# Kernel optimization log

Measured on AMD Instinct MI355X. Metric: run time of the kernel, lower is better.

Reference implementation:

```python
import jax, jax.numpy as jnp
import numpy as np

BN_EPS = 1e-5

def _bn_train(x, g, b):
    # BatchNorm1d in training mode: biased batch stats over the row dim
    m = x.mean(0)
    v = x.var(0)
    return g * (x - m) * jax.lax.rsqrt(v + BN_EPS) + b


def setup_inputs() -> dict:
    key = jax.random.key(0)
    ks = jax.random.split(key, 16)
    N, V, C, H, T, NC, OD, EH, EC = 128, 128, 256, 512, 12, 5, 5, 256, 256
    s = 0.05
    idx = jax.random.randint(ks[1], (T, N), 0, NC)
    return {
        "x": jax.random.normal(ks[0], (N, V, C), jnp.float32),
        "hidden_states": jnp.zeros((N, V, H), jnp.float32),
        "cell_states": jnp.zeros((N, V, H), jnp.float32),
        "one_hots_c_pred_seq": jax.nn.one_hot(idx, NC, dtype=jnp.float32),
        "W_ih": jax.random.normal(ks[2], (4 * H, C), jnp.float32) * s,
        "W_hh": jax.random.normal(ks[3], (4 * H, H), jnp.float32) * s,
        "b_ih": jax.random.normal(ks[4], (4 * H,), jnp.float32) * s,
        "b_hh": jax.random.normal(ks[5], (4 * H,), jnp.float32) * s,
        "W_cls": jax.random.normal(ks[6], (NC, H), jnp.float32) * s,
        "b_cls": jax.random.normal(ks[7], (NC,), jnp.float32) * s,
        "W_eh": jax.random.normal(ks[8], (EH, H), jnp.float32) * s,
        "b_eh": jax.random.normal(ks[9], (EH,), jnp.float32) * s,
        "g_eh": jnp.ones((EH,), jnp.float32),
        "beta_eh": jnp.zeros((EH,), jnp.float32),
        "W_ec": jax.random.normal(ks[10], (EC, NC), jnp.float32) * s,
        "b_ec": jax.random.normal(ks[11], (EC,), jnp.float32) * s,
        "g_ec": jnp.ones((EC,), jnp.float32),
        "beta_ec": jnp.zeros((EC,), jnp.float32),
        "W_out": jax.random.normal(ks[12], (OD, EH + EC), jnp.float32) * s,
        "b_out": jax.random.normal(ks[13], (OD,), jnp.float32) * s,
    }


def reference(x, hidden_states, cell_states, one_hots_c_pred_seq,
              W_ih, W_hh, b_ih, b_hh, W_cls, b_cls,
              W_eh, b_eh, g_eh, beta_eh, W_ec, b_ec, g_ec, beta_ec,
              W_out, b_out):
    N, V, C = x.shape
    H = hidden_states.shape[-1]
    xf = x.reshape(N * V, C)
    gx = xf @ W_ih.T + b_ih  # input gates are identical every step (x is repeated)

    def step(carry, onehot):
        h, c = carry  # [N*V, H]
        gates = gx + h @ W_hh.T + b_hh
        i, f, g, o = jnp.split(gates, 4, axis=1)  # pytorch LSTMCell gate order
        c = jax.nn.sigmoid(f) * c + jax.nn.sigmoid(i) * jnp.tanh(g)
        h = jax.nn.sigmoid(o) * jnp.tanh(c)
        # ClassifierLayer: avg-pool over V then 1x1 conv == mean + linear
        oc = h.reshape(N, V, H).mean(1) @ W_cls.T + b_cls  # [N, nc]
        # PredictionLayer
        eh = jax.nn.relu(_bn_train(h @ W_eh.T + b_eh, g_eh, beta_eh))
        ohr = jnp.broadcast_to(onehot[:, None, :], (N, V, onehot.shape[-1])).reshape(N * V, -1)
        ec = jax.nn.relu(_bn_train(ohr @ W_ec.T + b_ec, g_ec, beta_ec))
        op = jnp.concatenate([eh, ec], axis=1) @ W_out.T + b_out  # [N*V, out_dim]
        return (h, c), (op.reshape(N, V, -1), oc)

    carry0 = (hidden_states.reshape(N * V, H), cell_states.reshape(N * V, H))
    _, (preds, c_outs) = jax.lax.scan(step, carry0, one_hots_c_pred_seq)
    preds = preds.transpose(1, 0, 2, 3)  # [N, T, V, out_dim]
    # output_activation: bivariate-Gaussian params
    pred_outs = jnp.stack([preds[..., 0], preds[..., 1],
                           jnp.exp(preds[..., 2]), jnp.exp(preds[..., 3]),
                           jnp.tanh(preds[..., 4])], axis=-1)
    return pred_outs, c_outs
```

## Files before the change

kernel.cpp:

```cpp
#include <hip/hip_runtime.h>
#include <hip/hip_bf16.h>
#include <stdint.h>

typedef __hip_bfloat16 bf16;
typedef __attribute__((ext_vector_type(8))) short bf16x8;
typedef __attribute__((ext_vector_type(4))) short bf16x4;
typedef __attribute__((ext_vector_type(4))) float f32x4;

#define NN 128
#define VV 128
#define CC 256
#define HH 512
#define TT 12
#define NCLS 5
#define OD 5
#define EHD 256
#define KCAT (HH + CC)
#define ROWS (NN * VV)
#define PRED_SZ (NN * TT * VV * OD)
#define LDP 72
#define MiB (1ull << 20)


__device__ __forceinline__ float sigm(float x) { return 1.f / (1.f + __expf(-x)); }
__device__ __forceinline__ float tanh_(float x) {
    x = fminf(fmaxf(x, -15.f), 15.f);
    float e = __expf(2.f * x);
    return (e - 1.f) / (e + 1.f);
}
__device__ __forceinline__ float bf2f(unsigned short v) {
    unsigned u = ((unsigned)v) << 16; float f; __builtin_memcpy(&f, &u, 4); return f;
}
__device__ __forceinline__ float ldin(const void* p, int i, int is32) {
    return is32 ? ((const float*)p)[i] : __bfloat162float(((const bf16*)p)[i]);
}

__global__ void detect_dtype(const void* g_eh, int* flag, int* hnz) {
    unsigned w = *(const unsigned*)g_eh;
    *flag = (w == 0x3F800000u) ? 1 : 0;
    *hnz = 0;
}

__global__ __launch_bounds__(256) void convert_in(const void* src, bf16* dst, int n, const int* flag) {
    int is32 = *flag;
    int i = blockIdx.x * 256 + threadIdx.x;
    int stride = gridDim.x * 256;
    if (is32) { const float* s = (const float*)src; for (; i < n; i += stride) dst[i] = __float2bfloat16(s[i]); }
    else      { const bf16*  s = (const bf16*)src;  for (; i < n; i += stride) dst[i] = s[i]; }
}

__global__ __launch_bounds__(256) void convert_in_hflag(const void* src, bf16* dst, int n, const int* flag,
                                                        int* nz) {
    int is32 = *flag;
    int i = blockIdx.x * 256 + threadIdx.x;
    int stride = gridDim.x * 256;
    int loc = 0;
    if (is32) {
        const float* s = (const float*)src;
        for (; i < n; i += stride) { float v = s[i]; if (__float_as_uint(v) != 0u) loc = 1; dst[i] = __float2bfloat16(v); }
    } else {
        const bf16* s = (const bf16*)src;
        for (; i < n; i += stride) { bf16 v = s[i]; if (*(const unsigned short*)&v) loc = 1; dst[i] = v; }
    }
    if (loc) atomicOr(nz, 1);
}

__global__ __launch_bounds__(256) void init_c(const void* cell, bf16* c, const int* flag) {
    int is32 = *flag;
    size_t i = (size_t)blockIdx.x * 256 + threadIdx.x;
    const size_t total = (size_t)ROWS * HH;
    for (; i < total; i += (size_t)8192 * 256) c[i] = __float2bfloat16(ldin(cell, (int)i, is32));
}

__device__ __forceinline__ void issue_loads(const bf16* __restrict__ A, int lda, int row0, int ka,
                                            const bf16* __restrict__ B, int ldb, int col0, int kb,
                                            bf16x8 ar[4], bf16x8 br[4]) {
    int tid = threadIdx.x;
#pragma unroll
    for (int it = 0; it < 4; ++it) {
        int cidx = tid + 256 * it;
        int row = cidx >> 3;
        int cc8 = (cidx & 7) * 8;
        ar[it] = *(const bf16x8*)(A + (size_t)(row0 + row) * lda + ka + cc8);
        br[it] = *(const bf16x8*)(B + (size_t)(col0 + row) * ldb + kb + cc8);
    }
}
__device__ __forceinline__ void write_lds(bf16* As, bf16* Bs, const bf16x8 ar[4], const bf16x8 br[4]) {
    int tid = threadIdx.x;
#pragma unroll
    for (int it = 0; it < 4; ++it) {
        int cidx = tid + 256 * it;
        int row = cidx >> 3;
        int cc8 = (cidx & 7) * 8;
        *(bf16x8*)(As + row * LDP + cc8) = ar[it];
        *(bf16x8*)(Bs + row * LDP + cc8) = br[it];
    }
}
__device__ __forceinline__ void tile_mfma(const bf16* As, const bf16* Bs, f32x4 acc[4][4]) {
    const int lane = threadIdx.x & 63, wave = threadIdx.x >> 6;
    const int wro = (wave >> 1) * 64, wco = (wave & 1) * 64;
    const int l15 = lane & 15, l8 = (lane >> 4) * 8;
#pragma unroll
    for (int kk = 0; kk < 64; kk += 32) {
        bf16x8 af[4], bg[4];
#pragma unroll
        for (int x = 0; x < 4; ++x) {
            af[x] = *(const bf16x8*)(As + (wro + x * 16 + l15) * LDP + kk + l8);
            bg[x] = *(const bf16x8*)(Bs + (wco + x * 16 + l15) * LDP + kk + l8);
        }
#pragma unroll
        for (int bi = 0; bi < 4; ++bi)
#pragma unroll
            for (int bj = 0; bj < 4; ++bj)
                acc[bi][bj] = __builtin_amdgcn_mfma_f32_16x16x32_bf16(af[bi], bg[bj], acc[bi][bj], 0, 0, 0);
    }
}

__global__ __launch_bounds__(256) void prep_weights(const void* __restrict__ Wih, const void* __restrict__ Whh,
                                                    const void* __restrict__ bih, const void* __restrict__ bhh,
                                                    bf16* __restrict__ Wihp, bf16* __restrict__ Whhp,
                                                    float* __restrict__ biasp, const int* flag) {
    int is32 = *flag;
    int jg = blockIdx.x;
    int b = jg >> 7, j = jg & 127;
    int gate = (j >> 4) & 3;
    int unit = b * 32 + (j & 15) + 16 * (j >> 6);
    int p = gate * HH + unit;
    for (int k = threadIdx.x; k < HH; k += 256)
        Whhp[(size_t)jg * HH + k] = __float2bfloat16(ldin(Whh, p * HH + k, is32));
    for (int k = threadIdx.x; k < CC; k += 256)
        Wihp[(size_t)jg * CC + k] = __float2bfloat16(ldin(Wih, p * CC + k, is32));
    if (threadIdx.x == 0)
        biasp[jg] = ldin(bih, p, is32) + ldin(bhh, p, is32);
}

__global__ __launch_bounds__(256) void gemm_k0(const bf16* __restrict__ A, const bf16* __restrict__ B,
                                               const float* __restrict__ biasp, bf16* __restrict__ gx) {
    __shared__ bf16 As[128 * LDP], Bs[128 * LDP];
    f32x4 acc[4][4] = {};
    bf16x8 ar[4], br[4];
    int row0 = blockIdx.x * 128, col0 = blockIdx.y * 128;
    issue_loads(A, CC, row0, 0, B, CC, col0, 0, ar, br);
    for (int k0 = 0; k0 < CC; k0 += 64) {
        __syncthreads();
        write_lds(As, Bs, ar, br);
        __syncthreads();
        int kn = k0 + 64;
        if (kn < CC) issue_loads(A, CC, row0, kn, B, CC, col0, kn, ar, br);
        tile_mfma(As, Bs, acc);
    }
    int lane = threadIdx.x & 63, wave = threadIdx.x >> 6;
    int wro = (wave >> 1) * 64, wco = (wave & 1) * 64;
    int l15 = lane & 15, lr4 = (lane >> 4) * 4;
#pragma unroll
    for (int bj = 0; bj < 4; ++bj) {
        int j = wco + bj * 16 + l15;
        float bia = biasp[col0 + j];
        int sidx = wco + l15 * 4 + bj;
#pragma unroll
        for (int bi = 0; bi < 4; ++bi)
#pragma unroll
            for (int reg = 0; reg < 4; ++reg) {
                int r = row0 + wro + bi * 16 + lr4 + reg;
                gx[(size_t)r * 2048 + col0 + sidx] = __float2bfloat16(acc[bi][bj][reg] + bia);
            }
    }
}

__global__ __launch_bounds__(256) void ec_precompute(const void* __restrict__ W_ec, const void* __restrict__ b_ec,
                                                     const void* __restrict__ g_ec, const void* __restrict__ beta_ec,
                                                     const void* __restrict__ W_out, const void* __restrict__ b_out,
                                                     const void* __restrict__ onehot, float* __restrict__ ecd_all,
                                                     const int* flag) {
    __shared__ float ecv[NCLS][EHD];
    __shared__ float cntf[NCLS];
    __shared__ float ecdc[NCLS][OD];
    int is32 = *flag;
    int t = blockIdx.x, tid = threadIdx.x;
    int ohoff = t * NN * NCLS;
    if (tid < NCLS) {
        float cnum = 0.f;
        for (int n = 0; n < NN; ++n) cnum += ldin(onehot, ohoff + n * NCLS + tid, is32);
        cntf[tid] = cnum * (1.f / NN);
    }
    __syncthreads();
    {
        int j = tid;
        float vals[NCLS];
        float m = 0.f, e2 = 0.f;
        float be = ldin(b_ec, j, is32);
        for (int cc = 0; cc < NCLS; ++cc) {
            vals[cc] = ldin(W_ec, j * NCLS + cc, is32) + be;
            m += cntf[cc] * vals[cc];
            e2 += cntf[cc] * vals[cc] * vals[cc];
        }
        float rs = rsqrtf(e2 - m * m + 1e-5f);
        float g = ldin(g_ec, j, is32), bt = ldin(beta_ec, j, is32);
        for (int cc = 0; cc < NCLS; ++cc)
            ecv[cc][j] = fmaxf(g * (vals[cc] - m) * rs + bt, 0.f);
    }
    __syncthreads();
    if (tid < NCLS * OD) {
        int cc = tid / OD, k = tid % OD;
        float s = 0.f;
        for (int j = 0; j < EHD; ++j) s += ecv[cc][j] * ldin(W_out, k * (EHD * 2) + EHD + j, is32);
        ecdc[cc][k] = s;
    }
    __syncthreads();
    if (tid < NN) {
        for (int k = 0; k < OD; ++k) {
            float s = ldin(b_out, k, is32);
            for (int cc = 0; cc < NCLS; ++cc) s += ldin(onehot, ohoff + tid * NCLS + cc, is32) * ecdc[cc][k];
            ecd_all[((size_t)t * NN + tid) * OD + k] = s;
        }
    }
}

__device__ __forceinline__ void final_rows(int grp, const bf16* __restrict__ ehp, const float* __restrict__ colsum,
                                           const float* __restrict__ colss, const void* __restrict__ g_eh,
                                           const void* __restrict__ beta_eh, const float* __restrict__ ecd_all,
                                           const float* Wl, void* __restrict__ out, int t, int is32) {
    int wave = threadIdx.x >> 6, lane = threadIdx.x & 63;
    int r = grp * 4 + wave;
    int j0 = lane * 4;
    float av[4], bv[4];
#pragma unroll
    for (int e = 0; e < 4; ++e) {
        float mean = colsum[j0 + e] * (1.f / ROWS);
        float var = colss[j0 + e] * (1.f / ROWS) - mean * mean;
        float a = ldin(g_eh, j0 + e, is32) * rsqrtf(var + 1e-5f);
        av[e] = a;
        bv[e] = ldin(beta_eh, j0 + e, is32) - mean * a;
    }
    bf16x4 xs = *(const bf16x4*)(ehp + (size_t)r * EHD + j0);
    float v0 = fmaxf(av[0] * bf2f((unsigned short)xs[0]) + bv[0], 0.f);
    float v1 = fmaxf(av[1] * bf2f((unsigned short)xs[1]) + bv[1], 0.f);
    float v2 = fmaxf(av[2] * bf2f((unsigned short)xs[2]) + bv[2], 0.f);
    float v3 = fmaxf(av[3] * bf2f((unsigned short)xs[3]) + bv[3], 0.f);
    float p[OD];
#pragma unroll
    for (int k = 0; k < OD; ++k)
        p[k] = v0 * Wl[k * EHD + j0] + v1 * Wl[k * EHD + j0 + 1] + v2 * Wl[k * EHD + j0 + 2] + v3 * Wl[k * EHD + j0 + 3];
#pragma unroll
    for (int off = 32; off; off >>= 1)
#pragma unroll
        for (int k = 0; k < OD; ++k) p[k] += __shfl_down(p[k], off, 64);
    if (lane == 0) {
        int n = r >> 7, v = r & 127;
        const float* en = ecd_all + ((size_t)t * NN + n) * OD;
        float o0 = p[0] + en[0];
        float o1 = p[1] + en[1];
        float o2 = expf(p[2] + en[2]);
        float o3 = expf(p[3] + en[3]);
        float o4 = tanh_(p[4] + en[4]);
        size_t base = (size_t)n * (TT * VV * OD) + (size_t)t * (VV * OD) + (size_t)v * OD;
        if (is32) {
            float* dst = (float*)out + base;
            dst[0] = o0; dst[1] = o1; dst[2] = o2; dst[3] = o3; dst[4] = o4;
        } else {
            bf16* dst = (bf16*)out + base;
            dst[0] = __float2bfloat16(o0);
            dst[1] = __float2bfloat16(o1);
            dst[2] = __float2bfloat16(o2);
            dst[3] = __float2bfloat16(o3);
            dst[4] = __float2bfloat16(o4);
        }
    }
}

__global__ __launch_bounds__(256) void lstm_fused(const bf16* __restrict__ h_in, const bf16* __restrict__ Whhp,
                                                  const bf16* __restrict__ gx, bf16* __restrict__ c,
                                                  bf16* __restrict__ h_out, float* __restrict__ csum_cur,
                                                  float* __restrict__ colsum_z, float* __restrict__ colss_z,
                                                  const bf16* __restrict__ Weh, const void* __restrict__ b_eh,
                                                  bf16* __restrict__ ehp_w, float* __restrict__ colsum_w,
                                                  float* __restrict__ colss_w, const float* __restrict__ csum_prev,
                                                  const void* __restrict__ W_cls, const void* __restrict__ b_cls,
                                                  void* __restrict__ outp, int t_aux,
                                                  const bf16* __restrict__ ehp_r, const float* __restrict__ colsum_r,
                                                  const float* __restrict__ colss_r, const void* __restrict__ g_eh,
                                                  const void* __restrict__ beta_eh, const void* __restrict__ W_out,
                                                  const float* __restrict__ ecd_all, int t_final,
                                                  const int* __restrict__ flag) {
    __shared__ __align__(16) unsigned char smem[37376];
    int tid = threadIdx.x;
    if (blockIdx.x < 2048) {
        bf16* As = (bf16*)smem;
        bf16* Bs = (bf16*)(smem + 128 * LDP * 2);
        float* hsum = (float*)(smem + 36864);
        f32x4 acc[4][4] = {};
        bf16x8 ar[4], br[4];
        bf16x4 gpre[16];
        unsigned short cpre[16];
        int row0 = (blockIdx.x & 127) * 128, col0 = (blockIdx.x >> 7) * 128;
        int lane = tid & 63, wave = tid >> 6;
        int wro = (wave >> 1) * 64;
        int l15 = lane & 15, lr4 = (lane >> 4) * 4;
        int ul = (wave & 1) * 16 + l15;
        int u = (blockIdx.x >> 7) * 32 + ul;
        const bf16* gxp = gx + col0 + (wave & 1) * 64 + l15 * 4;
        issue_loads(h_in, HH, row0, 0, Whhp, HH, col0, 0, ar, br);
#pragma unroll
        for (int k0 = 0; k0 < HH; k0 += 64) {
            __syncthreads();
            write_lds(As, Bs, ar, br);
            __syncthreads();
            int kn = k0 + 64;
            if (kn < HH) issue_loads(h_in, HH, row0, kn, Whhp, HH, col0, kn, ar, br);
#pragma unroll
            for (int e = 0; e < 2; ++e) {
                int idx = (k0 >> 6) * 2 + e;
                int bi = idx >> 2, reg = idx & 3;
                int r = row0 + wro + bi * 16 + lr4 + reg;
                gpre[idx] = *(const bf16x4*)(gxp + (size_t)r * 2048);
                cpre[idx] = *(const unsigned short*)(c + (size_t)r * HH + u);
            }
            tile_mfma(As, Bs, acc);
        }
        if (tid < 32) hsum[tid] = 0.f;
        if (blockIdx.x == 0) { colsum_z[tid] = 0.f; colss_z[tid] = 0.f; }
        __syncthreads();
        float hpart = 0.f;
#pragma unroll
        for (int bi = 0; bi < 4; ++bi) {
#pragma unroll
            for (int reg = 0; reg < 4; ++reg) {
                int idx = bi * 4 + reg;
                int r = row0 + wro + bi * 16 + lr4 + reg;
                float gi = acc[bi][0][reg] + bf2f((unsigned short)gpre[idx][0]);
                float gf = acc[bi][1][reg] + bf2f((unsigned short)gpre[idx][1]);
                float gg = acc[bi][2][reg] + bf2f((unsigned short)gpre[idx][2]);
                float go = acc[bi][3][reg] + bf2f((unsigned short)gpre[idx][3]);
                float iv = sigm(gi), fv = sigm(gf), gv = tanh_(gg), ov = sigm(go);
                size_t ci = (size_t)r * HH + u;
                float cn = fv * bf2f(cpre[idx]) + iv * gv;
                c[ci] = __float2bfloat16(cn);
                float hv = ov * tanh_(cn);
                h_out[ci] = __float2bfloat16(hv);
                hpart += hv;
            }
        }
        atomicAdd(&hsum[ul], hpart);
        __syncthreads();
        if (tid < 32) csum_cur[(size_t)(blockIdx.x & 127) * HH + (blockIdx.x >> 7) * 32 + tid] = hsum[tid];
        return;
    }
    int is32 = *flag;
    int b = blockIdx.x - 2048;
    if (b >= 640) {
        if (t_final < 0) return;
        float* Wl = (float*)smem;
        for (int i = tid; i < OD * EHD; i += 256)
            Wl[i] = ldin(W_out, (i >> 8) * (EHD * 2) + (i & 255), is32);
        __syncthreads();
        int fb = b - 640;
#pragma unroll
        for (int g = 0; g < 4; ++g)
            final_rows(fb * 4 + g, ehp_r, colsum_r, colss_r, g_eh, beta_eh, ecd_all, Wl, outp, t_final, is32);
        return;
    }
    if (b >= 512) {
        if (t_aux < 0) return;
        float* wl = (float*)smem;
        float* wred = (float*)(smem + 10240);
        int wave = tid >> 6, lane = tid & 63;
        for (int i = tid; i < NCLS * HH; i += 256) wl[i] = ldin(W_cls, i, is32);
        __syncthreads();
        int n = b - 512;
        float pk[NCLS] = {};
        for (int u = tid; u < HH; u += 256) {
            float cv = csum_prev[(size_t)n * HH + u];
#pragma unroll
            for (int k = 0; k < NCLS; ++k) pk[k] += cv * wl[k * HH + u];
        }
#pragma unroll
        for (int off = 32; off; off >>= 1)
#pragma unroll
            for (int k = 0; k < NCLS; ++k) pk[k] += __shfl_down(pk[k], off, 64);
        if (lane == 0)
#pragma unroll
            for (int k = 0; k < NCLS; ++k) wred[wave * NCLS + k] = pk[k];
        __syncthreads();
        if (tid < NCLS) {
            float a = (wred[tid] + wred[NCLS + tid] + wred[2 * NCLS + tid] + wred[3 * NCLS + tid]) * (1.f / VV)
                      + ldin(b_cls, tid, is32);
            int idx = PRED_SZ + t_aux * (NN * NCLS) + n * NCLS + tid;
            if (is32) ((float*)outp)[idx] = a;
            else      ((bf16*)outp)[idx] = __float2bfloat16(a);
        }
        return;
    }
    if (t_aux < 0) return;
    bf16* As = (bf16*)smem;
    bf16* Bs = (bf16*)(smem + 9216);
    float* s_sum = (float*)(smem + 27648);
    float* s_ss  = (float*)(smem + 28160);
    f32x4 acc[4][2] = {};
    bf16x8 ar[2], br[4];
    int row0 = (b >> 1) * 64, col0 = (b & 1) * 128;
#pragma unroll
    for (int it = 0; it < 2; ++it) { int cx = tid + 256 * it; ar[it] = *(const bf16x8*)(h_in + (size_t)(row0 + (cx >> 3)) * HH + (cx & 7) * 8); }
#pragma unroll
    for (int it = 0; it < 4; ++it) { int cx = tid + 256 * it; br[it] = *(const bf16x8*)(Weh + (size_t)(col0 + (cx >> 3)) * HH + (cx & 7) * 8); }
    const int lane = tid & 63, wave = tid >> 6;
    const int l15 = lane & 15, l8 = (lane >> 4) * 8;
    for (int k0 = 0; k0 < HH; k0 += 64) {
        __syncthreads();
#pragma unroll
        for (int it = 0; it < 2; ++it) { int cx = tid + 256 * it; *(bf16x8*)(As + (cx >> 3) * LDP + (cx & 7) * 8) = ar[it]; }
#pragma unroll
        for (int it = 0; it < 4; ++it) { int cx = tid + 256 * it; *(bf16x8*)(Bs + (cx >> 3) * LDP + (cx & 7) * 8) = br[it]; }
        __syncthreads();
        int kn = k0 + 64;
        if (kn < HH) {
#pragma unroll
            for (int it = 0; it < 2; ++it) { int cx = tid + 256 * it; ar[it] = *(const bf16x8*)(h_in + (size_t)(row0 + (cx >> 3)) * HH + kn + (cx & 7) * 8); }
#pragma unroll
            for (int it = 0; it < 4; ++it) { int cx = tid + 256 * it; br[it] = *(const bf16x8*)(Weh + (size_t)(col0 + (cx >> 3)) * HH + kn + (cx & 7) * 8); }
        }
#pragma unroll
        for (int kk = 0; kk < 64; kk += 32) {
            bf16x8 af[4], bg[2];
#pragma unroll
            for (int x = 0; x < 4; ++x) af[x] = *(const bf16x8*)(As + (x * 16 + l15) * LDP + kk + l8);
#pragma unroll
            for (int x = 0; x < 2; ++x) bg[x] = *(const bf16x8*)(Bs + (wave * 32 + x * 16 + l15) * LDP + kk + l8);
#pragma unroll
            for (int bi = 0; bi < 4; ++bi)
#pragma unroll
                for (int bj = 0; bj < 2; ++bj)
                    acc[bi][bj] = __builtin_amdgcn_mfma_f32_16x16x32_bf16(af[bi], bg[bj], acc[bi][bj], 0, 0, 0);
        }
    }
    int lr4 = (lane >> 4) * 4;
    if (tid < 128) { s_sum[tid] = 0.f; s_ss[tid] = 0.f; }
    __syncthreads();
#pragma unroll
    for (int bj = 0; bj < 2; ++bj) {
        int j = wave * 32 + bj * 16 + l15;
        int col = col0 + j;
        float bia = ldin(b_eh, col, is32);
        float ps = 0.f, pss = 0.f;
#pragma unroll
        for (int bi = 0; bi < 4; ++bi)
#pragma unroll
            for (int reg = 0; reg < 4; ++reg) {
                int r = row0 + bi * 16 + lr4 + reg;
                float val = acc[bi][bj][reg] + bia;
                ehp_w[(size_t)r * EHD + col] = __float2bfloat16(val);
                ps += val; pss += val * val;
            }
        atomicAdd(&s_sum[j], ps);
        atomicAdd(&s_ss[j], pss);
    }
    __syncthreads();
    if (tid < 128) {
        atomicAdd(&colsum_w[col0 + tid], s_sum[tid]);
        atomicAdd(&colss_w[col0 + tid], s_ss[tid]);
    }
}

__global__ __launch_bounds__(256) void lstm_gemm_gx_first(const bf16* __restrict__ h_in, const bf16* __restrict__ Whhp,
                                                          const bf16* __restrict__ gx, bf16* __restrict__ c,
                                                          bf16* __restrict__ h_out, float* __restrict__ csum,
                                                          float* __restrict__ colsum, float* __restrict__ colss,
                                                          const int* __restrict__ gemm_flag) {
    __shared__ bf16 As[128 * LDP], Bs[128 * LDP];
    __shared__ float hsum[32];
    f32x4 acc[4][4] = {};
    bf16x8 ar[4], br[4];
    bf16x4 gpre[16];
    unsigned short cpre[16];
    int row0 = blockIdx.x * 128, col0 = blockIdx.y * 128;
    int tid = threadIdx.x, lane = tid & 63, wave = tid >> 6;
    int wro = (wave >> 1) * 64;
    int l15 = lane & 15, lr4 = (lane >> 4) * 4;
    int ul = (wave & 1) * 16 + l15;
    int u = blockIdx.y * 32 + ul;
    const bf16* gxp = gx + col0 + (wave & 1) * 64 + l15 * 4;
    const int do_gemm = *gemm_flag;
    if (do_gemm) {
        issue_loads(h_in, HH, row0, 0, Whhp, HH, col0, 0, ar, br);
#pragma unroll
        for (int k0 = 0; k0 < HH; k0 += 64) {
            __syncthreads();
            write_lds(As, Bs, ar, br);
            __syncthreads();
            int kn = k0 + 64;
            if (kn < HH) issue_loads(h_in, HH, row0, kn, Whhp, HH, col0, kn, ar, br);
#pragma unroll
            for (int e = 0; e < 2; ++e) {
                int idx = (k0 >> 6) * 2 + e;
                int bi = idx >> 2, reg = idx & 3;
                int r = row0 + wro + bi * 16 + lr4 + reg;
                gpre[idx] = *(const bf16x4*)(gxp + (size_t)r * 2048);
                cpre[idx] = *(const unsigned short*)(c + (size_t)r * HH + u);
            }
            tile_mfma(As, Bs, acc);
        }
    } else {
#pragma unroll
        for (int idx = 0; idx < 16; ++idx) {
            int bi = idx >> 2, reg = idx & 3;
            int r = row0 + wro + bi * 16 + lr4 + reg;
            gpre[idx] = *(const bf16x4*)(gxp + (size_t)r * 2048);
            cpre[idx] = *(const unsigned short*)(c + (size_t)r * HH + u);
        }
    }
    if (tid < 32) hsum[tid] = 0.f;
    if (blockIdx.x == 0 && blockIdx.y == 0) { colsum[tid] = 0.f; colss[tid] = 0.f; }
    __syncthreads();
    float hpart = 0.f;
#pragma unroll
    for (int bi = 0; bi < 4; ++bi) {
#pragma unroll
        for (int reg = 0; reg < 4; ++reg) {
            int idx = bi * 4 + reg;
            int r = row0 + wro + bi * 16 + lr4 + reg;
            float gi = acc[bi][0][reg] + bf2f((unsigned short)gpre[idx][0]);
            float gf = acc[bi][1][reg] + bf2f((unsigned short)gpre[idx][1]);
            float gg = acc[bi][2][reg] + bf2f((unsigned short)gpre[idx][2]);
            float go = acc[bi][3][reg] + bf2f((unsigned short)gpre[idx][3]);
            float iv = sigm(gi), fv = sigm(gf), gv = tanh_(gg), ov = sigm(go);
            size_t ci = (size_t)r * HH + u;
            float cn = fv * bf2f(cpre[idx]) + iv * gv;
            c[ci] = __float2bfloat16(cn);
            float hv = ov * tanh_(cn);
            h_out[ci] = __float2bfloat16(hv);
            hpart += hv;
        }
    }
    atomicAdd(&hsum[ul], hpart);
    __syncthreads();
    if (tid < 32) csum[(size_t)blockIdx.x * HH + blockIdx.y * 32 + tid] = hsum[tid];
}

__global__ __launch_bounds__(256) void lstm_gemm_cat(const bf16* __restrict__ h_in, const bf16* __restrict__ x,
                                                     const bf16* __restrict__ Wihp, const bf16* __restrict__ Whhp,
                                                     const float* __restrict__ biasp, bf16* __restrict__ c,
                                                     bf16* __restrict__ h_out, float* __restrict__ csum,
                                                     float* __restrict__ colsum, float* __restrict__ colss) {
    __shared__ bf16 As[128 * LDP], Bs[128 * LDP];
    __shared__ float hsum[32];
    f32x4 acc[4][4] = {};
    bf16x8 ar[4], br[4];
    int row0 = blockIdx.x * 128, col0 = blockIdx.y * 128;
    issue_loads(h_in, HH, row0, 0, Whhp, HH, col0, 0, ar, br);
    for (int k0 = 0; k0 < KCAT; k0 += 64) {
        __syncthreads();
        write_lds(As, Bs, ar, br);
        __syncthreads();
        int kn = k0 + 64;
        if (kn < KCAT) {
            if (kn < HH) issue_loads(h_in, HH, row0, kn, Whhp, HH, col0, kn, ar, br);
            else         issue_loads(x, CC, row0, kn - HH, Wihp, CC, col0, kn - HH, ar, br);
        }
        tile_mfma(As, Bs, acc);
    }
    int tid = threadIdx.x;
    if (tid < 32) hsum[tid] = 0.f;
    if (blockIdx.x == 0 && blockIdx.y == 0) { colsum[tid] = 0.f; colss[tid] = 0.f; }
    __syncthreads();
    int lane = tid & 63, wave = tid >> 6;
    int wro = (wave >> 1) * 64;
    int l15 = lane & 15, lr4 = (lane >> 4) * 4;
    int ul = (wave & 1) * 16 + l15;
    int u = blockIdx.y * 32 + ul;
    int colp = col0 + (wave & 1) * 64 + l15;
    float b0 = biasp[colp], b1 = biasp[colp + 16], b2 = biasp[colp + 32], b3 = biasp[colp + 48];
    float hpart = 0.f;
#pragma unroll
    for (int bi = 0; bi < 4; ++bi) {
#pragma unroll
        for (int reg = 0; reg < 4; ++reg) {
            int r = row0 + wro + bi * 16 + lr4 + reg;
            float gi = acc[bi][0][reg] + b0;
            float gf = acc[bi][1][reg] + b1;
            float gg = acc[bi][2][reg] + b2;
            float go = acc[bi][3][reg] + b3;
            float iv = sigm(gi), fv = sigm(gf), gv = tanh_(gg), ov = sigm(go);
            size_t ci = (size_t)r * HH + u;
            float cn = fv * __bfloat162float(c[ci]) + iv * gv;
            c[ci] = __float2bfloat16(cn);
            float hv = ov * tanh_(cn);
            h_out[ci] = __float2bfloat16(hv);
            hpart += hv;
        }
    }
    atomicAdd(&hsum[ul], hpart);
    __syncthreads();
    if (tid < 32) csum[(size_t)blockIdx.x * HH + blockIdx.y * 32 + tid] = hsum[tid];
}

__global__ __launch_bounds__(256) void eh_cls(const bf16* __restrict__ A, const bf16* __restrict__ B,
                                              const void* __restrict__ bias, bf16* __restrict__ out,
                                              float* __restrict__ colsum, float* __restrict__ colss,
                                              const float* __restrict__ csum, const void* __restrict__ W_cls,
                                              const void* __restrict__ b_cls, void* __restrict__ outp,
                                              int t, const int* flag,
                                              const bf16* __restrict__ ehp_prev, const float* __restrict__ colsum_prev,
                                              const float* __restrict__ colss_prev, const void* __restrict__ g_eh,
                                              const void* __restrict__ beta_eh, const void* __restrict__ W_out,
                                              const float* __restrict__ ecd_all, int tprev) {
    __shared__ __align__(16) unsigned char smem[37376];
    int is32 = *flag;
    int tid = threadIdx.x;
    if (blockIdx.x >= 640) {
        if (tprev < 0) return;
        float* Wl = (float*)smem;
        for (int i = tid; i < OD * EHD; i += 256)
            Wl[i] = ldin(W_out, (i >> 8) * (EHD * 2) + (i & 255), is32);
        __syncthreads();
        int fb = blockIdx.x - 640;
#pragma unroll
        for (int g = 0; g < 4; ++g)
            final_rows(fb * 4 + g, ehp_prev, colsum_prev, colss_prev, g_eh, beta_eh,
                       ecd_all, Wl, outp, tprev, is32);
        return;
    }
    if (blockIdx.x >= 512) {
        float* wl = (float*)smem;
        float* wred = (float*)(smem + 10240);
        int wave = tid >> 6, lane = tid & 63;
        for (int i = tid; i < NCLS * HH; i += 256) wl[i] = ldin(W_cls, i, is32);
        __syncthreads();
        int n = blockIdx.x - 512;
        float pk[NCLS] = {};
        for (int u = tid; u < HH; u += 256) {
            float cv = csum[(size_t)n * HH + u];
#pragma unroll
            for (int k = 0; k < NCLS; ++k) pk[k] += cv * wl[k * HH + u];
        }
#pragma unroll
        for (int off = 32; off; off >>= 1)
#pragma unroll
            for (int k = 0; k < NCLS; ++k) pk[k] += __shfl_down(pk[k], off, 64);
        if (lane == 0)
#pragma unroll
            for (int k = 0; k < NCLS; ++k) wred[wave * NCLS + k] = pk[k];
        __syncthreads();
        if (tid < NCLS) {
            float a = (wred[tid] + wred[NCLS + tid] + wred[2 * NCLS + tid] + wred[3 * NCLS + tid]) * (1.f / VV)
                      + ldin(b_cls, tid, is32);
            int idx = PRED_SZ + t * (NN * NCLS) + n * NCLS + tid;
            if (is32) ((float*)outp)[idx] = a;
            else      ((bf16*)outp)[idx] = __float2bfloat16(a);
        }
        return;
    }
    bf16* As = (bf16*)smem;
    bf16* Bs = (bf16*)(smem + 9216);
    float* s_sum = (float*)(smem + 27648);
    float* s_ss  = (float*)(smem + 28160);
    f32x4 acc[4][2] = {};
    bf16x8 ar[2], br[4];
    int row0 = (blockIdx.x >> 1) * 64, col0 = (blockIdx.x & 1) * 128;
#pragma unroll
    for (int it = 0; it < 2; ++it) { int cx = tid + 256 * it; ar[it] = *(const bf16x8*)(A + (size_t)(row0 + (cx >> 3)) * HH + (cx & 7) * 8); }
#pragma unroll
    for (int it = 0; it < 4; ++it) { int cx = tid + 256 * it; br[it] = *(const bf16x8*)(B + (size_t)(col0 + (cx >> 3)) * HH + (cx & 7) * 8); }
    const int lane = tid & 63, wave = tid >> 6;
    const int l15 = lane & 15, l8 = (lane >> 4) * 8;
    for (int k0 = 0; k0 < HH; k0 += 64) {
        __syncthreads();
#pragma unroll
        for (int it = 0; it < 2; ++it) { int cx = tid + 256 * it; *(bf16x8*)(As + (cx >> 3) * LDP + (cx & 7) * 8) = ar[it]; }
#pragma unroll
        for (int it = 0; it < 4; ++it) { int cx = tid + 256 * it; *(bf16x8*)(Bs + (cx >> 3) * LDP + (cx & 7) * 8) = br[it]; }
        __syncthreads();
        int kn = k0 + 64;
        if (kn < HH) {
#pragma unroll
            for (int it = 0; it < 2; ++it) { int cx = tid + 256 * it; ar[it] = *(const bf16x8*)(A + (size_t)(row0 + (cx >> 3)) * HH + kn + (cx & 7) * 8); }
#pragma unroll
            for (int it = 0; it < 4; ++it) { int cx = tid + 256 * it; br[it] = *(const bf16x8*)(B + (size_t)(col0 + (cx >> 3)) * HH + kn + (cx & 7) * 8); }
        }
#pragma unroll
        for (int kk = 0; kk < 64; kk += 32) {
            bf16x8 af[4], bg[2];
#pragma unroll
            for (int x = 0; x < 4; ++x) af[x] = *(const bf16x8*)(As + (x * 16 + l15) * LDP + kk + l8);
#pragma unroll
            for (int x = 0; x < 2; ++x) bg[x] = *(const bf16x8*)(Bs + (wave * 32 + x * 16 + l15) * LDP + kk + l8);
#pragma unroll
            for (int bi = 0; bi < 4; ++bi)
#pragma unroll
                for (int bj = 0; bj < 2; ++bj)
                    acc[bi][bj] = __builtin_amdgcn_mfma_f32_16x16x32_bf16(af[bi], bg[bj], acc[bi][bj], 0, 0, 0);
        }
    }
    int lr4 = (lane >> 4) * 4;
    if (tid < 128) { s_sum[tid] = 0.f; s_ss[tid] = 0.f; }
    __syncthreads();
#pragma unroll
    for (int bj = 0; bj < 2; ++bj) {
        int j = wave * 32 + bj * 16 + l15;
        int col = col0 + j;
        float bia = ldin(bias, col, is32);
        float ps = 0.f, pss = 0.f;
#pragma unroll
        for (int bi = 0; bi < 4; ++bi)
#pragma unroll
            for (int reg = 0; reg < 4; ++reg) {
                int r = row0 + bi * 16 + lr4 + reg;
                float val = acc[bi][bj][reg] + bia;
                out[(size_t)r * EHD + col] = __float2bfloat16(val);
                ps += val; pss += val * val;
            }
        atomicAdd(&s_sum[j], ps);
        atomicAdd(&s_ss[j], pss);
    }
    __syncthreads();
    if (tid < 128) {
        atomicAdd(&colsum[col0 + tid], s_sum[tid]);
        atomicAdd(&colss[col0 + tid], s_ss[tid]);
    }
}

__global__ __launch_bounds__(256) void final_kernel(const bf16* __restrict__ eh_pre, const float* __restrict__ colsum,
                                                    const float* __restrict__ colss, const void* __restrict__ g_eh,
                                                    const void* __restrict__ beta_eh, const void* __restrict__ W_out,
                                                    const float* __restrict__ ecd_all, void* __restrict__ out,
                                                    int t, const int* flag) {
    __shared__ float Wl[OD * EHD];
    int is32 = *flag;
    for (int i = threadIdx.x; i < OD * EHD; i += 256)
        Wl[i] = ldin(W_out, (i >> 8) * (EHD * 2) + (i & 255), is32);
    __syncthreads();
    final_rows(blockIdx.x, eh_pre, colsum, colss, g_eh, beta_eh, ecd_all, Wl, out, t, is32);
}

extern "C" void kernel_launch(void* const* d_in, const int* in_sizes, int n_in,
                              void* d_out, int out_size, void* d_ws, size_t ws_size,
                              hipStream_t stream) {
    const void* x       = d_in[0];
    const void* hidden  = d_in[1];
    const void* cell    = d_in[2];
    const void* onehot  = d_in[3];
    const void* W_ih    = d_in[4];
    const void* W_hh    = d_in[5];
    const void* b_ih    = d_in[6];
    const void* b_hh    = d_in[7];
    const void* W_cls   = d_in[8];
    const void* b_cls   = d_in[9];
    const void* W_eh    = d_in[10];
    const void* b_eh    = d_in[11];
    const void* g_eh    = d_in[12];
    const void* beta_eh = d_in[13];
    const void* W_ec    = d_in[14];
    const void* b_ec    = d_in[15];
    const void* g_ec    = d_in[16];
    const void* beta_ec = d_in[17];
    const void* W_out   = d_in[18];
    const void* b_out   = d_in[19];

    const int use_gx = (ws_size >= 148 * MiB) ? 1 : 0;

    char* ws = (char*)d_ws;
    bf16*  cbuf = (bf16*)(ws);
    char*  tail = ws + 16 * MiB;
    bf16*  h0   = (bf16*)(ws + 32 * MiB);
    bf16*  h1   = (bf16*)(ws + 48 * MiB);
    bf16*  gxb  = (bf16*)(ws + 64 * MiB);
    bf16*  ehp0, *ehp1, *x_c, *Wihp, *Whhp, *Weh_c;
    if (use_gx) {
        ehp0  = (bf16*)(ws + 128 * MiB);
        x_c   = (bf16*)(ws + 136 * MiB);
        ehp1  = (bf16*)(ws + 136 * MiB);
        Wihp  = (bf16*)(ws + 144 * MiB);
        Whhp  = (bf16*)(ws + 145 * MiB);
        Weh_c = (bf16*)(ws + 147 * MiB);
    } else {
        ehp0  = (bf16*)(ws + 64 * MiB);
        x_c   = (bf16*)(ws + 72 * MiB);
        ehp1  = (bf16*)(ws + 80 * MiB);
        Wihp  = (bf16*)(ws + 88 * MiB);
        Whhp  = (bf16*)(ws + 89 * MiB);
        Weh_c = (bf16*)(ws + 91 * MiB);
    }
    float* biasp   = (float*)(tail);
    float* colsum3[3] = { (float*)(tail + 8192), (float*)(tail + 10240), (float*)(tail + 12288) };
    float* colss3[3]  = { (float*)(tail + 9216), (float*)(tail + 11264), (float*)(tail + 13312) };
    int*   dflag   = (int*)  (tail + 16384);
    int*   hnz     = (int*)  (tail + 16388);
    float* csum0   = (float*)(tail + 20480);
    float* csum1   = (float*)(tail + 20480 + 262144);
    float* ecd_all = (float*)(tail + 20480 + 524288);

    bf16*  ehp_b[2]  = { ehp0, ehp1 };
    float* csum_b[2] = { csum0, csum1 };

    detect_dtype<<<1, 1, 0, stream>>>(g_eh, dflag, hnz);
    convert_in<<<4096, 256, 0, stream>>>(x, x_c, ROWS * CC, dflag);
    convert_in_hflag<<<4096, 256, 0, stream>>>(hidden, h0, ROWS * HH, dflag, hnz);
    convert_in<<<512, 256, 0, stream>>>(W_eh, Weh_c, EHD * HH, dflag);
    init_c<<<8192, 256, 0, stream>>>(cell, cbuf, dflag);
    prep_weights<<<2048, 256, 0, stream>>>(W_ih, W_hh, b_ih, b_hh, Wihp, Whhp, biasp, dflag);
    ec_precompute<<<TT, 256, 0, stream>>>(W_ec, b_ec, g_ec, beta_ec, W_out, b_out, onehot, ecd_all, dflag);
    if (use_gx)
        gemm_k0<<<dim3(128, 16), 256, 0, stream>>>(x_c, Wihp, biasp, gxb);

    if (use_gx) {
        lstm_gemm_gx_first<<<dim3(128, 16), 256, 0, stream>>>(h0, Whhp, gxb, cbuf, h1, csum_b[0],
                                                              colsum3[0], colss3[0], hnz);
        for (int t = 1; t < TT; ++t) {
            const bf16* hin = (t & 1) ? h1 : h0;
            bf16* hout = (t & 1) ? h0 : h1;
            int tp = t - 1, tf = t - 2;
            lstm_fused<<<3712, 256, 0, stream>>>(
                hin, Whhp, gxb, cbuf, hout, csum_b[t & 1], colsum3[t % 3], colss3[t % 3],
                Weh_c, b_eh, ehp_b[tp & 1], colsum3[tp % 3], colss3[tp % 3], csum_b[tp & 1],
                W_cls, b_cls, d_out, tp,
                ehp_b[t & 1] , colsum3[(tf + 3) % 3], colss3[(tf + 3) % 3],
                g_eh, beta_eh, W_out, ecd_all, tf, dflag);
        }
        {
            int t = TT - 1;
            const bf16* h_last = (t & 1) ? h1 : h0;
            eh_cls<<<1664, 256, 0, stream>>>(h_last, Weh_c, b_eh, ehp_b[t & 1], colsum3[t % 3], colss3[t % 3],
                                             csum_b[t & 1], W_cls, b_cls, d_out, t, dflag,
                                             ehp_b[(t - 1) & 1], colsum3[(t - 1) % 3], colss3[(t - 1) % 3],
                                             g_eh, beta_eh, W_out, ecd_all, t - 1);
            final_kernel<<<4096, 256, 0, stream>>>(ehp_b[t & 1], colsum3[t % 3], colss3[t % 3],
                                                   g_eh, beta_eh, W_out, ecd_all, d_out, t, dflag);
        }
    } else {
        for (int t = 0; t < TT; ++t) {
            const bf16* hin = (t & 1) ? h1 : h0;
            bf16* hout = (t & 1) ? h0 : h1;
            lstm_gemm_cat<<<dim3(128, 16), 256, 0, stream>>>(hin, x_c, Wihp, Whhp, biasp, cbuf, hout,
                                                             csum_b[t & 1], colsum3[t % 3], colss3[t % 3]);
            eh_cls<<<1664, 256, 0, stream>>>(hout, Weh_c, b_eh, ehp_b[t & 1], colsum3[t % 3], colss3[t % 3],
                                             csum_b[t & 1], W_cls, b_cls, d_out, t, dflag,
                                             ehp_b[(t - 1) & 1], colsum3[((t - 1) + 3) % 3], colss3[((t - 1) + 3) % 3],
                                             g_eh, beta_eh, W_out, ecd_all, t - 1);
        }
        final_kernel<<<4096, 256, 0, stream>>>(ehp_b[(TT - 1) & 1], colsum3[(TT - 1) % 3], colss3[(TT - 1) % 3],
                                               g_eh, beta_eh, W_out, ecd_all, d_out, TT - 1, dflag);
    }
}
```

Baseline: 1.193 ms.

## Stage GEMM tiles via direct global-to-LDS loads and use fast reciprocal activations

Replaces register-staged global→LDS tile copies in all GEMM kernels with global_load_lds direct transfers into an unpadded 64-wide LDS layout. This removes the register round-trip and VGPR pressure and shrinks shared memory per block. It also drops the register prefetch of the next k-tile, so the load for each tile is no longer overlapped with MFMA work. The unpadded stride may also cause LDS bank conflicts on fragment reads. Sigmoid and tanh now use hardware reciprocal instead of division.

Result: slower. 1.222 ms (+2.4%).

```diff
diff --git a/kernel.cpp b/kernel.cpp
--- a/kernel.cpp
+++ b/kernel.cpp
@@ -22,17 +22,58 @@
 #define MiB (1ull << 20)
 
 
-__device__ __forceinline__ float sigm(float x) { return 1.f / (1.f + __expf(-x)); }
+__device__ __forceinline__ float sigm(float x) {
+    return __builtin_amdgcn_rcpf(1.f + __expf(-x));
+}
 __device__ __forceinline__ float tanh_(float x) {
     x = fminf(fmaxf(x, -15.f), 15.f);
     float e = __expf(2.f * x);
-    return (e - 1.f) / (e + 1.f);
+    return (e - 1.f) * __builtin_amdgcn_rcpf(e + 1.f);
 }
 __device__ __forceinline__ float bf2f(unsigned short v) {
     unsigned u = ((unsigned)v) << 16; float f; __builtin_memcpy(&f, &u, 4); return f;
 }
 __device__ __forceinline__ float ldin(const void* p, int i, int is32) {
     return is32 ? ((const float*)p)[i] : __bfloat162float(((const bf16*)p)[i]);
+}
+
+__device__ __forceinline__ void gl_lds16(const bf16* g, bf16* l) {
+    __builtin_amdgcn_global_load_lds(
+        (const __attribute__((address_space(1))) unsigned int*)g,
+        (__attribute__((address_space(3))) unsigned int*)l, 16, 0, 0);
+}
+__device__ __forceinline__ void stage128(const bf16* __restrict__ A, int lda, int row0,
+                                         const bf16* __restrict__ B, int ldb, int col0,
+                                         int k, bf16* As, bf16* Bs) {
+    int lane = threadIdx.x & 63, wave = threadIdx.x >> 6;
+    const bf16* pA = A + (size_t)(row0 + wave * 32 + (lane >> 3)) * lda + k + (lane & 7) * 8;
+    const bf16* pB = B + (size_t)(col0 + wave * 32 + (lane >> 3)) * ldb + k + (lane & 7) * 8;
+    bf16* lA = As + wave * 2048 + lane * 8;
+    bf16* lB = Bs + wave * 2048 + lane * 8;
+#pragma unroll
+    for (int j = 0; j < 4; ++j) {
+        gl_lds16(pA + (size_t)(j * 8) * lda, lA + j * 512);
+        gl_lds16(pB + (size_t)(j * 8) * ldb, lB + j * 512);
+    }
+}
+__device__ __forceinline__ void tile_mfma64(const bf16* As, const bf16* Bs, f32x4 acc[4][4]) {
+    const int lane = threadIdx.x & 63, wave = threadIdx.x >> 6;
+    const int wro = (wave >> 1) * 64, wco = (wave & 1) * 64;
+    const int l15 = lane & 15, l8 = (lane >> 4) * 8;
+#pragma unroll
+    for (int kk = 0; kk < 64; kk += 32) {
+        bf16x8 af[4], bg[4];
+#pragma unroll
+        for (int x = 0; x < 4; ++x) {
+            af[x] = *(const bf16x8*)(As + (wro + x * 16 + l15) * 64 + kk + l8);
+            bg[x] = *(const bf16x8*)(Bs + (wco + x * 16 + l15) * 64 + kk + l8);
+        }
+#pragma unroll
+        for (int bi = 0; bi < 4; ++bi)
+#pragma unroll
+            for (int bj = 0; bj < 4; ++bj)
+                acc[bi][bj] = __builtin_amdgcn_mfma_f32_16x16x32_bf16(af[bi], bg[bj], acc[bi][bj], 0, 0, 0);
+    }
 }
 
 __global__ void detect_dtype(const void* g_eh, int* flag, int* hnz) {
@@ -136,18 +177,14 @@
 
 __global__ __launch_bounds__(256) void gemm_k0(const bf16* __restrict__ A, const bf16* __restrict__ B,
                                                const float* __restrict__ biasp, bf16* __restrict__ gx) {
-    __shared__ bf16 As[128 * LDP], Bs[128 * LDP];
+    __shared__ bf16 As[128 * 64], Bs[128 * 64];
     f32x4 acc[4][4] = {};
-    bf16x8 ar[4], br[4];
     int row0 = blockIdx.x * 128, col0 = blockIdx.y * 128;
-    issue_loads(A, CC, row0, 0, B, CC, col0, 0, ar, br);
     for (int k0 = 0; k0 < CC; k0 += 64) {
         __syncthreads();
-        write_lds(As, Bs, ar, br);
-        __syncthreads();
-        int kn = k0 + 64;
-        if (kn < CC) issue_loads(A, CC, row0, kn, B, CC, col0, kn, ar, br);
-        tile_mfma(As, Bs, acc);
+        stage128(A, CC, row0, B, CC, col0, k0, As, Bs);
+        __syncthreads();
+        tile_mfma64(As, Bs, acc);
     }
     int lane = threadIdx.x & 63, wave = threadIdx.x >> 6;
     int wro = (wave >> 1) * 64, wco = (wave & 1) * 64;
@@ -282,14 +319,12 @@
                                                   const void* __restrict__ beta_eh, const void* __restrict__ W_out,
                                                   const float* __restrict__ ecd_all, int t_final,
                                                   const int* __restrict__ flag) {
-    __shared__ __align__(16) unsigned char smem[37376];
+    __shared__ __align__(16) unsigned char smem[32768];
     int tid = threadIdx.x;
     if (blockIdx.x < 2048) {
         bf16* As = (bf16*)smem;
-        bf16* Bs = (bf16*)(smem + 128 * LDP * 2);
-        float* hsum = (float*)(smem + 36864);
+        bf16* Bs = (bf16*)(smem + 16384);
         f32x4 acc[4][4] = {};
-        bf16x8 ar[4], br[4];
         bf16x4 gpre[16];
         unsigned short cpre[16];
         int row0 = (blockIdx.x & 127) * 128, col0 = (blockIdx.x >> 7) * 128;
@@ -299,14 +334,11 @@
         int ul = (wave & 1) * 16 + l15;
         int u = (blockIdx.x >> 7) * 32 + ul;
         const bf16* gxp = gx + col0 + (wave & 1) * 64 + l15 * 4;
-        issue_loads(h_in, HH, row0, 0, Whhp, HH, col0, 0, ar, br);
 #pragma unroll
         for (int k0 = 0; k0 < HH; k0 += 64) {
             __syncthreads();
-            write_lds(As, Bs, ar, br);
+            stage128(h_in, HH, row0, Whhp, HH, col0, k0, As, Bs);
             __syncthreads();
-            int kn = k0 + 64;
-            if (kn < HH) issue_loads(h_in, HH, row0, kn, Whhp, HH, col0, kn, ar, br);
 #pragma unroll
             for (int e = 0; e < 2; ++e) {
                 int idx = (k0 >> 6) * 2 + e;
@@ -315,8 +347,10 @@
                 gpre[idx] = *(const bf16x4*)(gxp + (size_t)r * 2048);
                 cpre[idx] = *(const unsigned short*)(c + (size_t)r * HH + u);
             }
-            tile_mfma(As, Bs, acc);
-        }
+            tile_mfma64(As, Bs, acc);
+        }
+        __syncthreads();
+        float* hsum = (float*)smem;
         if (tid < 32) hsum[tid] = 0.f;
         if (blockIdx.x == 0) { colsum_z[tid] = 0.f; colss_z[tid] = 0.f; }
         __syncthreads();
@@ -392,39 +426,31 @@
     }
     if (t_aux < 0) return;
     bf16* As = (bf16*)smem;
-    bf16* Bs = (bf16*)(smem + 9216);
-    float* s_sum = (float*)(smem + 27648);
-    float* s_ss  = (float*)(smem + 28160);
+    bf16* Bs = (bf16*)(smem + 8192);
+    float* s_sum = (float*)(smem + 24576);
+    float* s_ss  = (float*)(smem + 25088);
     f32x4 acc[4][2] = {};
-    bf16x8 ar[2], br[4];
     int row0 = (b >> 1) * 64, col0 = (b & 1) * 128;
-#pragma unroll
-    for (int it = 0; it < 2; ++it) { int cx = tid + 256 * it; ar[it] = *(const bf16x8*)(h_in + (size_t)(row0 + (cx >> 3)) * HH + (cx & 7) * 8); }
-#pragma unroll
-    for (int it = 0; it < 4; ++it) { int cx = tid + 256 * it; br[it] = *(const bf16x8*)(Weh + (size_t)(col0 + (cx >> 3)) * HH + (cx & 7) * 8); }
     const int lane = tid & 63, wave = tid >> 6;
     const int l15 = lane & 15, l8 = (lane >> 4) * 8;
+    const bf16* pA = h_in + (size_t)(row0 + wave * 16 + (lane >> 3)) * HH + (lane & 7) * 8;
+    const bf16* pB = Weh + (size_t)(col0 + wave * 32 + (lane >> 3)) * HH + (lane & 7) * 8;
+    bf16* lA = As + wave * 1024 + lane * 8;
+    bf16* lB = Bs + wave * 2048 + lane * 8;
     for (int k0 = 0; k0 < HH; k0 += 64) {
         __syncthreads();
-#pragma unroll
-        for (int it = 0; it < 2; ++it) { int cx = tid + 256 * it; *(bf16x8*)(As + (cx >> 3) * LDP + (cx & 7) * 8) = ar[it]; }
-#pragma unroll
-        for (int it = 0; it < 4; ++it) { int cx = tid + 256 * it; *(bf16x8*)(Bs + (cx >> 3) * LDP + (cx & 7) * 8) = br[it]; }
-        __syncthreads();
-        int kn = k0 + 64;
-        if (kn < HH) {
-#pragma unroll
-            for (int it = 0; it < 2; ++it) { int cx = tid + 256 * it; ar[it] = *(const bf16x8*)(h_in + (size_t)(row0 + (cx >> 3)) * HH + kn + (cx & 7) * 8); }
-#pragma unroll
-            for (int it = 0; it < 4; ++it) { int cx = tid + 256 * it; br[it] = *(const bf16x8*)(Weh + (size_t)(col0 + (cx >> 3)) * HH + kn + (cx & 7) * 8); }
-        }
+        gl_lds16(pA + k0, lA);
+        gl_lds16(pA + 8 * HH + k0, lA + 512);
+#pragma unroll
+        for (int j = 0; j < 4; ++j) gl_lds16(pB + (size_t)(j * 8) * HH + k0, lB + j * 512);
+        __syncthreads();
 #pragma unroll
         for (int kk = 0; kk < 64; kk += 32) {
             bf16x8 af[4], bg[2];
 #pragma unroll
-            for (int x = 0; x < 4; ++x) af[x] = *(const bf16x8*)(As + (x * 16 + l15) * LDP + kk + l8);
-#pragma unroll
-            for (int x = 0; x < 2; ++x) bg[x] = *(const bf16x8*)(Bs + (wave * 32 + x * 16 + l15) * LDP + kk + l8);
+            for (int x = 0; x < 4; ++x) af[x] = *(const bf16x8*)(As + (x * 16 + l15) * 64 + kk + l8);
+#pragma unroll
+            for (int x = 0; x < 2; ++x) bg[x] = *(const bf16x8*)(Bs + (wave * 32 + x * 16 + l15) * 64 + kk + l8);
 #pragma unroll
             for (int bi = 0; bi < 4; ++bi)
 #pragma unroll
@@ -465,10 +491,9 @@
                                                           bf16* __restrict__ h_out, float* __restrict__ csum,
                                                           float* __restrict__ colsum, float* __restrict__ colss,
                                                           const int* __restrict__ gemm_flag) {
-    __shared__ bf16 As[128 * LDP], Bs[128 * LDP];
+    __shared__ bf16 As[128 * 64], Bs[128 * 64];
     __shared__ float hsum[32];
     f32x4 acc[4][4] = {};
-    bf16x8 ar[4], br[4];
     bf16x4 gpre[16];
     unsigned short cpre[16];
     int row0 = blockIdx.x * 128, col0 = blockIdx.y * 128;
@@ -480,14 +505,11 @@
     const bf16* gxp = gx + col0 + (wave & 1) * 64 + l15 * 4;
     const int do_gemm = *gemm_flag;
     if (do_gemm) {
-        issue_loads(h_in, HH, row0, 0, Whhp, HH, col0, 0, ar, br);
 #pragma unroll
         for (int k0 = 0; k0 < HH; k0 += 64) {
             __syncthreads();
-            write_lds(As, Bs, ar, br);
+            stage128(h_in, HH, row0, Whhp, HH, col0, k0, As, Bs);
             __syncthreads();
-            int kn = k0 + 64;
-            if (kn < HH) issue_loads(h_in, HH, row0, kn, Whhp, HH, col0, kn, ar, br);
 #pragma unroll
             for (int e = 0; e < 2; ++e) {
                 int idx = (k0 >> 6) * 2 + e;
@@ -496,7 +518,7 @@
                 gpre[idx] = *(const bf16x4*)(gxp + (size_t)r * 2048);
                 cpre[idx] = *(const unsigned short*)(c + (size_t)r * HH + u);
             }
-            tile_mfma(As, Bs, acc);
+            tile_mfma64(As, Bs, acc);
         }
     } else {
 #pragma unroll
@@ -507,6 +529,7 @@
             cpre[idx] = *(const unsigned short*)(c + (size_t)r * HH + u);
         }
     }
+    __syncthreads();
     if (tid < 32) hsum[tid] = 0.f;
     if (blockIdx.x == 0 && blockIdx.y == 0) { colsum[tid] = 0.f; colss[tid] = 0.f; }
     __syncthreads();
@@ -602,7 +625,7 @@
                                               const float* __restrict__ colss_prev, const void* __restrict__ g_eh,
                                               const void* __restrict__ beta_eh, const void* __restrict__ W_out,
                                               const float* __restrict__ ecd_all, int tprev) {
-    __shared__ __align__(16) unsigned char smem[37376];
+    __shared__ __align__(16) unsigned char smem[32768];
     int is32 = *flag;
     int tid = threadIdx.x;
     if (blockIdx.x >= 640) {
@@ -649,39 +672,31 @@
         return;
     }
     bf16* As = (bf16*)smem;
-    bf16* Bs = (bf16*)(smem + 9216);
-    float* s_sum = (float*)(smem + 27648);
-    float* s_ss  = (float*)(smem + 28160);
+    bf16* Bs = (bf16*)(smem + 8192);
+    float* s_sum = (float*)(smem + 24576);
+    float* s_ss  = (float*)(smem + 25088);
     f32x4 acc[4][2] = {};
-    bf16x8 ar[2], br[4];
     int row0 = (blockIdx.x >> 1) * 64, col0 = (blockIdx.x & 1) * 128;
-#pragma unroll
-    for (int it = 0; it < 2; ++it) { int cx = tid + 256 * it; ar[it] = *(const bf16x8*)(A + (size_t)(row0 + (cx >> 3)) * HH + (cx & 7) * 8); }
-#pragma unroll
-    for (int it = 0; it < 4; ++it) { int cx = tid + 256 * it; br[it] = *(const bf16x8*)(B + (size_t)(col0 + (cx >> 3)) * HH + (cx & 7) * 8); }
     const int lane = tid & 63, wave = tid >> 6;
     const int l15 = lane & 15, l8 = (lane >> 4) * 8;
+    const bf16* pA = A + (size_t)(row0 + wave * 16 + (lane >> 3)) * HH + (lane & 7) * 8;
+    const bf16* pB = B + (size_t)(col0 + wave * 32 + (lane >> 3)) * HH + (lane & 7) * 8;
+    bf16* lA = As + wave * 1024 + lane * 8;
+    bf16* lB = Bs + wave * 2048 + lane * 8;
     for (int k0 = 0; k0 < HH; k0 += 64) {
         __syncthreads();
-#pragma unroll
-        for (int it = 0; it < 2; ++it) { int cx = tid + 256 * it; *(bf16x8*)(As + (cx >> 3) * LDP + (cx & 7) * 8) = ar[it]; }
-#pragma unroll
-        for (int it = 0; it < 4; ++it) { int cx = tid + 256 * it; *(bf16x8*)(Bs + (cx >> 3) * LDP + (cx & 7) * 8) = br[it]; }
-        __syncthreads();
-        int kn = k0 + 64;
-        if (kn < HH) {
-#pragma unroll
-            for (int it = 0; it < 2; ++it) { int cx = tid + 256 * it; ar[it] = *(const bf16x8*)(A + (size_t)(row0 + (cx >> 3)) * HH + kn + (cx & 7) * 8); }
-#pragma unroll
-            for (int it = 0; it < 4; ++it) { int cx = tid + 256 * it; br[it] = *(const bf16x8*)(B + (size_t)(col0 + (cx >> 3)) * HH + kn + (cx & 7) * 8); }
-        }
+        gl_lds16(pA + k0, lA);
+        gl_lds16(pA + 8 * HH + k0, lA + 512);
+#pragma unroll
+        for (int j = 0; j < 4; ++j) gl_lds16(pB + (size_t)(j * 8) * HH + k0, lB + j * 512);
+        __syncthreads();
 #pragma unroll
         for (int kk = 0; kk < 64; kk += 32) {
             bf16x8 af[4], bg[2];
 #pragma unroll
-            for (int x = 0; x < 4; ++x) af[x] = *(const bf16x8*)(As + (x * 16 + l15) * LDP + kk + l8);
-#pragma unroll
-            for (int x = 0; x < 2; ++x) bg[x] = *(const bf16x8*)(Bs + (wave * 32 + x * 16 + l15) * LDP + kk + l8);
+            for (int x = 0; x < 4; ++x) af[x] = *(const bf16x8*)(As + (x * 16 + l15) * 64 + kk + l8);
+#pragma unroll
+            for (int x = 0; x < 2; ++x) bg[x] = *(const bf16x8*)(Bs + (wave * 32 + x * 16 + l15) * 64 + kk + l8);
 #pragma unroll
             for (int bi = 0; bi < 4; ++bi)
 #pragma unroll
```
